# Kernel optimization log

Measured on AMD Instinct MI355X. Metric: run time of the kernel, lower is better.

The kernel has to match this reference:

```python
import jax, jax.numpy as jnp
import numpy as np

NUM_EXPERTS = 8
TOP_K = 2


def setup_inputs() -> dict:
    key = jax.random.key(0)
    ks = jax.random.split(key, 5)
    B, T, D, H, E = 8, 4096, 512, 1536, NUM_EXPERTS
    scale = 0.02
    x = jax.random.normal(ks[0], (B, T, D), dtype=jnp.float32)
    gate_w = jax.random.normal(ks[1], (E, D), dtype=jnp.float32) * scale
    w1 = jax.random.normal(ks[2], (E, H, D), dtype=jnp.float32) * scale
    w3 = jax.random.normal(ks[3], (E, H, D), dtype=jnp.float32) * scale
    w2 = jax.random.normal(ks[4], (E, D, H), dtype=jnp.float32) * scale
    return {"x": x, "gate_w": gate_w, "w1": w1, "w3": w3, "w2": w2}


def reference(x, gate_w, w1, w3, w2):
    B, T, D = x.shape
    E = gate_w.shape[0]
    xf = x.reshape(-1, D)                      # [N, D], N = B*T
    N = xf.shape[0]
    gate_logits = xf @ gate_w.T                # [N, E]
    weights, indices = jax.lax.top_k(gate_logits, TOP_K)   # [N, K]
    weights = jax.nn.softmax(weights, axis=-1)
    # combine[n, e] = sum_k weights[n, k] * (indices[n, k] == e)
    combine = jnp.zeros((N, E), dtype=xf.dtype).at[
        jnp.arange(N)[:, None], indices].add(weights)       # [N, E]
    out = jnp.zeros_like(xf)
    for e in range(E):  # small fixed expert count
        h = jax.nn.silu(xf @ w1[e].T) * (xf @ w3[e].T)      # [N, H]
        y = h @ w2[e].T                                     # [N, D]
        out = out + combine[:, e:e + 1] * y
    return out.reshape(B, T, D)
```

## Files before the change

### kernel.cpp

```cpp
#include <hip/hip_runtime.h>


#define N_TOK 32768
#define DIM   512
#define HID   1536
#define NE    8
#define MTS   256

typedef __attribute__((ext_vector_type(8))) short  short8;
typedef __attribute__((ext_vector_type(4))) float  floatx4;

#define MFMA(a,b,c) __builtin_amdgcn_mfma_f32_16x16x32_bf16(a,b,c,0,0,0)

__device__ __forceinline__ unsigned short f2bf(float f) {
  unsigned int u = __float_as_uint(f);
  u += 0x7fffu + ((u >> 16) & 1u);
  return (unsigned short)(u >> 16);
}
__device__ __forceinline__ unsigned pk2(float a, float b) {
  return (unsigned)f2bf(a) | ((unsigned)f2bf(b) << 16);
}
__device__ __forceinline__ void gl_lds16(const unsigned short* g, unsigned short* l) {
  __builtin_amdgcn_global_load_lds(
      (const __attribute__((address_space(1))) unsigned int*)g,
      (__attribute__((address_space(3))) unsigned int*)l, 16, 0, 0);
}

__global__ void __launch_bounds__(256) cvt_kernel(const float* __restrict__ src,
                                                  unsigned short* __restrict__ dst,
                                                  int n4) {
  int i = blockIdx.x * 256 + threadIdx.x;
  if (i >= n4) return;
  float4 v = ((const float4*)src)[i];
  uint2 o; o.x = pk2(v.x, v.y); o.y = pk2(v.z, v.w);
  ((uint2*)dst)[i] = o;
}

__global__ void __launch_bounds__(256) gate1_kernel(const float* __restrict__ x,
                                                    const float* __restrict__ gw,
                                                    unsigned short* __restrict__ xb,
                                                    unsigned* __restrict__ eidx,
                                                    float* __restrict__ wts) {
  int lane = threadIdx.x & 63;
  int wave = threadIdx.x >> 6;
  int t = blockIdx.x * 4 + wave;

  const float4* xp = (const float4*)(x + (size_t)t * DIM + lane * 8);
  float4 x0 = xp[0], x1 = xp[1];

  uint4 o; o.x = pk2(x0.x, x0.y); o.y = pk2(x0.z, x0.w);
  o.z = pk2(x1.x, x1.y); o.w = pk2(x1.z, x1.w);
  *(uint4*)(xb + (size_t)t * DIM + lane * 8) = o;

  double p[NE];
#pragma unroll
  for (int e = 0; e < NE; ++e) {
    const float4* gp = (const float4*)(gw + e * DIM + lane * 8);
    float4 g0 = gp[0], g1 = gp[1];
    p[e] = (double)x0.x * g0.x + (double)x0.y * g0.y + (double)x0.z * g0.z + (double)x0.w * g0.w
         + (double)x1.x * g1.x + (double)x1.y * g1.y + (double)x1.z * g1.z + (double)x1.w * g1.w;
  }
#pragma unroll
  for (int m = 1; m < 64; m <<= 1) {
#pragma unroll
    for (int e = 0; e < NE; ++e) p[e] += __shfl_xor(p[e], m);
  }
  if (lane == 0) {
    double m1 = -1e300, m2 = -1e300; int i1 = 0, i2 = 0;
#pragma unroll
    for (int e = 0; e < NE; ++e) {
      double v = p[e];
      if (v > m1) { m2 = m1; i2 = i1; m1 = v; i1 = e; }
      else if (v > m2) { m2 = v; i2 = e; }
    }
    float e2 = __expf((float)(m2 - m1));
    float wa = 1.f / (1.f + e2);
    eidx[t] = (unsigned)i1 | ((unsigned)i2 << 8);
    wts[t]  = wa;
  }
}

__global__ void __launch_bounds__(256) gate2_kernel(const unsigned* __restrict__ eidx,
                                                    const float* __restrict__ wts,
                                                    int* __restrict__ tokl,
                                                    float* __restrict__ wgtl,
                                                    int* __restrict__ cnt) {
  __shared__ unsigned hist[NE];
  __shared__ unsigned basep[NE];
  int tid = threadIdx.x;
  if (tid < NE) hist[tid] = 0;
  __syncthreads();
  int t0 = blockIdx.x * 1024;
  unsigned pk[4]; float wv[4];
#pragma unroll
  for (int i = 0; i < 4; ++i) {
    int t = t0 + tid + i * 256;
    pk[i] = eidx[t]; wv[i] = wts[t];
    atomicAdd(&hist[pk[i] & 0xff], 1u);
    atomicAdd(&hist[(pk[i] >> 8) & 0xff], 1u);
  }
  __syncthreads();
  if (tid < NE) {
    basep[tid] = (unsigned)atomicAdd(&cnt[tid], (int)hist[tid]);
    hist[tid] = 0;
  }
  __syncthreads();
#pragma unroll
  for (int i = 0; i < 4; ++i) {
    int t = t0 + tid + i * 256;
    int e1 = pk[i] & 0xff, e2 = (pk[i] >> 8) & 0xff;
    unsigned p1 = basep[e1] + atomicAdd(&hist[e1], 1u);
    tokl[e1 * N_TOK + p1] = t; wgtl[e1 * N_TOK + p1] = wv[i];
    unsigned p2 = basep[e2] + atomicAdd(&hist[e2], 1u);
    tokl[e2 * N_TOK + p2] = t | (int)0x80000000; wgtl[e2 * N_TOK + p2] = 1.f - wv[i];
  }
}

__global__ void __launch_bounds__(256, 4) ffn1_kernel(
    const unsigned short* __restrict__ xb,
    const unsigned short* __restrict__ w1b,
    const unsigned short* __restrict__ w3b,
    const int* __restrict__ tokl, const float* __restrict__ wgtl,
    const int* __restrict__ cnt,
    unsigned short* __restrict__ Hs,
    int h0base, int P, int NT) {
  int e  = blockIdx.x & 7;
  int t  = blockIdx.x >> 3;
  int nt = t % NT, mt = t / NT;
  int ne = cnt[e];
  int m0 = mt * 128;
  if (m0 >= ne) return;
  int offs = 0;
#pragma unroll
  for (int i = 0; i < NE; ++i) offs += (i < e) ? cnt[i] : 0;

  __shared__ __align__(16) unsigned short As[128 * 64];
  __shared__ __align__(16) unsigned short Bs[128 * 64];
  __shared__ float wgs[128];

  int tid = threadIdx.x, w = tid >> 6, lane = tid & 63;
  int quad = lane >> 4, l16 = lane & 15;
  int wm = w >> 1, wn = w & 1;

  if (tid < 128) {
    int r = m0 + tid;
    wgs[tid] = (r < ne) ? wgtl[e * N_TOK + r] : 0.f;
  }

  int rl = lane >> 3, cc = (lane & 7) ^ rl;
  const unsigned short* pa[4];
#pragma unroll
  for (int i = 0; i < 4; ++i) {
    int r = m0 + 32 * w + 8 * i + rl;
    int tok = tokl[e * N_TOK + (r < ne ? r : m0)] & 0x7fffffff;
    pa[i] = xb + (size_t)tok * DIM + cc * 8;
  }
  const unsigned short* wsrc = (w < 2) ? w1b : w3b;
  const unsigned short* pb0 =
      wsrc + ((size_t)e * HID + h0base + nt * 64 + ((32 * w) & 63) + rl) * DIM + cc * 8;

  floatx4 u[4][2], v[4][2];
#pragma unroll
  for (int i = 0; i < 4; ++i)
#pragma unroll
    for (int j = 0; j < 2; ++j) { u[i][j] = (floatx4){0,0,0,0}; v[i][j] = (floatx4){0,0,0,0}; }

  for (int k0 = 0; k0 < DIM; k0 += 64) {
#pragma unroll
    for (int i = 0; i < 4; ++i) {
      gl_lds16(pa[i], &As[(32 * w + 8 * i) * 64]);
      gl_lds16(pb0 + (size_t)i * 8 * DIM, &Bs[(32 * w + 8 * i) * 64]);
      pa[i] += 64;
    }
    pb0 += 64;
    __syncthreads();
#pragma unroll
    for (int kk = 0; kk < 2; ++kk) {
      int s = ((4 * kk + quad) ^ (l16 & 7)) * 8;
      short8 a[4], b1[2], b3[2];
#pragma unroll
      for (int i = 0; i < 4; ++i)
        a[i] = *(const short8*)&As[(wm * 64 + i * 16 + l16) * 64 + s];
#pragma unroll
      for (int j = 0; j < 2; ++j) {
        b1[j] = *(const short8*)&Bs[(wn * 32 + j * 16 + l16) * 64 + s];
        b3[j] = *(const short8*)&Bs[(64 + wn * 32 + j * 16 + l16) * 64 + s];
      }
#pragma unroll
      for (int i = 0; i < 4; ++i)
#pragma unroll
        for (int j = 0; j < 2; ++j) {
          u[i][j] = MFMA(a[i], b1[j], u[i][j]);
          v[i][j] = MFMA(a[i], b3[j], v[i][j]);
        }
    }
    __syncthreads();
  }

#pragma unroll
  for (int i = 0; i < 4; ++i)
#pragma unroll
    for (int j = 0; j < 2; ++j)
#pragma unroll
      for (int r = 0; r < 4; ++r) {
        int tr = wm * 64 + i * 16 + quad * 4 + r;
        int hc = wn * 32 + j * 16 + l16;
        float uu = u[i][j][r], vv = v[i][j][r];
        float h = (uu / (1.f + __expf(-uu))) * vv * wgs[tr];
        As[tr * 64 + hc] = f2bf(h);
      }
  __syncthreads();
  {
    int row = tid >> 1, half = tid & 1;
    if (m0 + row < ne) {
      const unsigned short* s = &As[row * 64 + half * 32];
      unsigned short* d = Hs + (size_t)(offs + m0 + row) * P + nt * 64 + half * 32;
#pragma unroll
      for (int j = 0; j < 4; ++j) *(uint4*)(d + j * 8) = *(const uint4*)(s + j * 8);
    }
  }
}

__global__ void __launch_bounds__(256, 4) ffn2_kernel(
    const unsigned short* __restrict__ Hs,
    const unsigned short* __restrict__ w2b,
    const int* __restrict__ tokl, const int* __restrict__ cnt,
    float* __restrict__ out, float* __restrict__ prt,
    int h0base, int P, int first) {
  int e  = blockIdx.x & 7;
  int t  = blockIdx.x >> 3;
  int nt = t & 3, mt = t >> 2;
  int ne = cnt[e];
  int m0 = mt * 128;
  if (m0 >= ne) return;
  int offs = 0;
#pragma unroll
  for (int i = 0; i < NE; ++i) offs += (i < e) ? cnt[i] : 0;

  __shared__ __align__(16) unsigned short As[128 * 64];
  __shared__ __align__(16) unsigned short Bs[128 * 64];
  __shared__ int toks[128];

  int tid = threadIdx.x, w = tid >> 6, lane = tid & 63;
  int quad = lane >> 4, l16 = lane & 15;
  int wm = w >> 1, wn = w & 1;
  if (tid < 128) { int r = m0 + tid; toks[tid] = tokl[e * N_TOK + (r < ne ? r : m0)]; }

  int rl = lane >> 3, cc = (lane & 7) ^ rl;
  int dbase = nt * 128;
  const unsigned short* pa0 = Hs + (size_t)(offs + m0 + 32 * w + rl) * P + cc * 8;
  const unsigned short* pb0 =
      w2b + ((size_t)e * DIM + dbase + 32 * w + rl) * HID + h0base + cc * 8;

  floatx4 acc[4][4];
#pragma unroll
  for (int i = 0; i < 4; ++i)
#pragma unroll
    for (int j = 0; j < 4; ++j) acc[i][j] = (floatx4){0,0,0,0};

  for (int k0 = 0; k0 < P; k0 += 64) {
#pragma unroll
    for (int i = 0; i < 4; ++i) {
      gl_lds16(pa0 + (size_t)i * 8 * P,   &As[(32 * w + 8 * i) * 64]);
      gl_lds16(pb0 + (size_t)i * 8 * HID, &Bs[(32 * w + 8 * i) * 64]);
    }
    pa0 += 64; pb0 += 64;
    __syncthreads();
#pragma unroll
    for (int kk = 0; kk < 2; ++kk) {
      int s = ((4 * kk + quad) ^ (l16 & 7)) * 8;
      short8 a[4], b[4];
#pragma unroll
      for (int i = 0; i < 4; ++i) {
        a[i] = *(const short8*)&As[(wm * 64 + i * 16 + l16) * 64 + s];
        b[i] = *(const short8*)&Bs[(wn * 64 + i * 16 + l16) * 64 + s];
      }
#pragma unroll
      for (int i = 0; i < 4; ++i)
#pragma unroll
        for (int j = 0; j < 4; ++j)
          acc[i][j] = MFMA(a[i], b[j], acc[i][j]);
    }
    __syncthreads();
  }

#pragma unroll
  for (int i = 0; i < 4; ++i)
#pragma unroll
    for (int r = 0; r < 4; ++r) {
      int row = wm * 64 + i * 16 + quad * 4 + r;
      if (m0 + row >= ne) continue;
      int tk = toks[row];
      float* dst = ((tk < 0) ? prt : out)
                   + (size_t)(tk & 0x7fffffff) * DIM + dbase + wn * 64 + l16;
      if (first) {
#pragma unroll
        for (int j = 0; j < 4; ++j) dst[j * 16] = acc[i][j][r];
      } else {
#pragma unroll
        for (int j = 0; j < 4; ++j) dst[j * 16] += acc[i][j][r];
      }
    }
}

__global__ void __launch_bounds__(256) combine_kernel(float* __restrict__ out,
                                                      const float* __restrict__ prt,
                                                      int n4) {
  for (int i = blockIdx.x * 256 + threadIdx.x; i < n4; i += gridDim.x * 256) {
    float4 a = ((const float4*)out)[i];
    float4 b = ((const float4*)prt)[i];
    a.x += b.x; a.y += b.y; a.z += b.z; a.w += b.w;
    ((float4*)out)[i] = a;
  }
}

extern "C" void kernel_launch(void* const* d_in, const int* in_sizes, int n_in,
                              void* d_out, int out_size, void* d_ws, size_t ws_size,
                              hipStream_t stream) {
  const float* x  = (const float*)d_in[0];
  const float* gw = (const float*)d_in[1];
  const float* w1 = (const float*)d_in[2];
  const float* w3 = (const float*)d_in[3];
  const float* w2 = (const float*)d_in[4];
  float* out = (float*)d_out;

  const size_t NW = (size_t)NE * HID * DIM;
  char* p = (char*)d_ws;
  unsigned short* w1b = (unsigned short*)p;  p += NW * 2;
  unsigned short* w3b = (unsigned short*)p;  p += NW * 2;
  unsigned short* w2b = (unsigned short*)p;  p += NW * 2;
  unsigned short* xb  = (unsigned short*)p;  p += (size_t)N_TOK * DIM * 2;
  int*      tokl = (int*)p;       p += (size_t)NE * N_TOK * 4;
  float*    wgtl = (float*)p;     p += (size_t)NE * N_TOK * 4;
  unsigned* eidx = (unsigned*)p;  p += (size_t)N_TOK * 4;
  float*    wts  = (float*)p;     p += (size_t)N_TOK * 4;
  int*      cnt  = (int*)p;       p += 256;
  float*    prt  = (float*)p;     p += (size_t)N_TOK * DIM * 4;
  unsigned short* Hs = (unsigned short*)p;
  size_t fixed = (size_t)(p - (char*)d_ws);
  if (ws_size < fixed) return;
  size_t avail = ws_size - fixed;

  const int cands[5] = {1536, 768, 512, 384, 256};
  int P = 0;
  for (int i = 0; i < 5; ++i)
    if ((size_t)(2 * N_TOK + 128) * cands[i] * 2 <= avail) { P = cands[i]; break; }
  if (!P) return;

  hipMemsetAsync(cnt, 0, NE * sizeof(int), stream);

  int n4 = (int)(NW / 4);
  cvt_kernel<<<n4 / 256, 256, 0, stream>>>(w1, w1b, n4);
  cvt_kernel<<<n4 / 256, 256, 0, stream>>>(w3, w3b, n4);
  cvt_kernel<<<n4 / 256, 256, 0, stream>>>(w2, w2b, n4);

  gate1_kernel<<<N_TOK / 4, 256, 0, stream>>>(x, gw, xb, eidx, wts);
  gate2_kernel<<<N_TOK / 1024, 256, 0, stream>>>(eidx, wts, tokl, wgtl, cnt);

  int pass = 0;
  for (int h0 = 0; h0 < HID; h0 += P) {
    int NT = P / 64;
    ffn1_kernel<<<8 * MTS * NT, 256, 0, stream>>>(xb, w1b, w3b, tokl, wgtl, cnt, Hs, h0, P, NT);
    ffn2_kernel<<<8 * MTS * 4, 256, 0, stream>>>(Hs, w2b, tokl, cnt, out, prt, h0, P, pass == 0);
    ++pass;
  }
  combine_kernel<<<2048, 256, 0, stream>>>(out, prt, N_TOK * DIM / 4);
}
```

Measured before the change: 686.6 us.

## Double-buffer LDS tiles in FFN kernels to overlap global loads with MFMA

```diff
diff --git a/kernel.cpp b/kernel.cpp
--- a/kernel.cpp
+++ b/kernel.cpp
@@ -116,7 +116,7 @@
   }
 }
 
-__global__ void __launch_bounds__(256, 4) ffn1_kernel(
+__global__ void __launch_bounds__(256, 2) ffn1_kernel(
     const unsigned short* __restrict__ xb,
     const unsigned short* __restrict__ w1b,
     const unsigned short* __restrict__ w3b,
@@ -134,8 +134,8 @@
 #pragma unroll
   for (int i = 0; i < NE; ++i) offs += (i < e) ? cnt[i] : 0;
 
-  __shared__ __align__(16) unsigned short As[128 * 64];
-  __shared__ __align__(16) unsigned short Bs[128 * 64];
+  __shared__ __align__(16) unsigned short As[2][128 * 64];
+  __shared__ __align__(16) unsigned short Bs[2][128 * 64];
   __shared__ float wgs[128];
 
   int tid = threadIdx.x, w = tid >> 6, lane = tid & 63;
@@ -159,32 +159,44 @@
   const unsigned short* pb0 =
       wsrc + ((size_t)e * HID + h0base + nt * 64 + ((32 * w) & 63) + rl) * DIM + cc * 8;
 
+  auto stage = [&](int b) {
+#pragma unroll
+    for (int i = 0; i < 4; ++i) {
+      gl_lds16(pa[i], &As[b][(32 * w + 8 * i) * 64]);
+      gl_lds16(pb0 + (size_t)i * 8 * DIM, &Bs[b][(32 * w + 8 * i) * 64]);
+      pa[i] += 64;
+    }
+    pb0 += 64;
+  };
+
   floatx4 u[4][2], v[4][2];
 #pragma unroll
   for (int i = 0; i < 4; ++i)
 #pragma unroll
     for (int j = 0; j < 2; ++j) { u[i][j] = (floatx4){0,0,0,0}; v[i][j] = (floatx4){0,0,0,0}; }
 
+  stage(0);
+  int cur = 0;
+#pragma unroll
   for (int k0 = 0; k0 < DIM; k0 += 64) {
-#pragma unroll
-    for (int i = 0; i < 4; ++i) {
-      gl_lds16(pa[i], &As[(32 * w + 8 * i) * 64]);
-      gl_lds16(pb0 + (size_t)i * 8 * DIM, &Bs[(32 * w + 8 * i) * 64]);
-      pa[i] += 64;
-    }
-    pb0 += 64;
-    __syncthreads();
+    if (k0 + 64 < DIM) {
+      stage(cur ^ 1);
+      asm volatile("s_waitcnt vmcnt(8)" ::: "memory");
+    } else {
+      asm volatile("s_waitcnt vmcnt(0)" ::: "memory");
+    }
+    __builtin_amdgcn_s_barrier();
 #pragma unroll
     for (int kk = 0; kk < 2; ++kk) {
       int s = ((4 * kk + quad) ^ (l16 & 7)) * 8;
       short8 a[4], b1[2], b3[2];
 #pragma unroll
       for (int i = 0; i < 4; ++i)
-        a[i] = *(const short8*)&As[(wm * 64 + i * 16 + l16) * 64 + s];
+        a[i] = *(const short8*)&As[cur][(wm * 64 + i * 16 + l16) * 64 + s];
 #pragma unroll
       for (int j = 0; j < 2; ++j) {
-        b1[j] = *(const short8*)&Bs[(wn * 32 + j * 16 + l16) * 64 + s];
-        b3[j] = *(const short8*)&Bs[(64 + wn * 32 + j * 16 + l16) * 64 + s];
+        b1[j] = *(const short8*)&Bs[cur][(wn * 32 + j * 16 + l16) * 64 + s];
+        b3[j] = *(const short8*)&Bs[cur][(64 + wn * 32 + j * 16 + l16) * 64 + s];
       }
 #pragma unroll
       for (int i = 0; i < 4; ++i)
@@ -194,7 +206,9 @@
           v[i][j] = MFMA(a[i], b3[j], v[i][j]);
         }
     }
-    __syncthreads();
+    asm volatile("" ::: "memory");
+    __builtin_amdgcn_s_barrier();
+    cur ^= 1;
   }
 
 #pragma unroll
@@ -207,13 +221,13 @@
         int hc = wn * 32 + j * 16 + l16;
         float uu = u[i][j][r], vv = v[i][j][r];
         float h = (uu / (1.f + __expf(-uu))) * vv * wgs[tr];
-        As[tr * 64 + hc] = f2bf(h);
+        As[0][tr * 64 + hc] = f2bf(h);
       }
   __syncthreads();
   {
     int row = tid >> 1, half = tid & 1;
     if (m0 + row < ne) {
-      const unsigned short* s = &As[row * 64 + half * 32];
+      const unsigned short* s = &As[0][row * 64 + half * 32];
       unsigned short* d = Hs + (size_t)(offs + m0 + row) * P + nt * 64 + half * 32;
 #pragma unroll
       for (int j = 0; j < 4; ++j) *(uint4*)(d + j * 8) = *(const uint4*)(s + j * 8);
@@ -221,7 +235,7 @@
   }
 }
 
-__global__ void __launch_bounds__(256, 4) ffn2_kernel(
+__global__ void __launch_bounds__(256, 2) ffn2_kernel(
     const unsigned short* __restrict__ Hs,
     const unsigned short* __restrict__ w2b,
     const int* __restrict__ tokl, const int* __restrict__ cnt,
@@ -237,8 +251,8 @@
 #pragma unroll
   for (int i = 0; i < NE; ++i) offs += (i < e) ? cnt[i] : 0;
 
-  __shared__ __align__(16) unsigned short As[128 * 64];
-  __shared__ __align__(16) unsigned short Bs[128 * 64];
+  __shared__ __align__(16) unsigned short As[2][128 * 64];
+  __shared__ __align__(16) unsigned short Bs[2][128 * 64];
   __shared__ int toks[128];
 
   int tid = threadIdx.x, w = tid >> 6, lane = tid & 63;
@@ -252,28 +266,39 @@
   const unsigned short* pb0 =
       w2b + ((size_t)e * DIM + dbase + 32 * w + rl) * HID + h0base + cc * 8;
 
+  auto stage = [&](int b) {
+#pragma unroll
+    for (int i = 0; i < 4; ++i) {
+      gl_lds16(pa0 + (size_t)i * 8 * P,   &As[b][(32 * w + 8 * i) * 64]);
+      gl_lds16(pb0 + (size_t)i * 8 * HID, &Bs[b][(32 * w + 8 * i) * 64]);
+    }
+    pa0 += 64; pb0 += 64;
+  };
+
   floatx4 acc[4][4];
 #pragma unroll
   for (int i = 0; i < 4; ++i)
 #pragma unroll
     for (int j = 0; j < 4; ++j) acc[i][j] = (floatx4){0,0,0,0};
 
+  stage(0);
+  int cur = 0;
   for (int k0 = 0; k0 < P; k0 += 64) {
-#pragma unroll
-    for (int i = 0; i < 4; ++i) {
-      gl_lds16(pa0 + (size_t)i * 8 * P,   &As[(32 * w + 8 * i) * 64]);
-      gl_lds16(pb0 + (size_t)i * 8 * HID, &Bs[(32 * w + 8 * i) * 64]);
-    }
-    pa0 += 64; pb0 += 64;
-    __syncthreads();
+    if (k0 + 64 < P) {
+      stage(cur ^ 1);
+      asm volatile("s_waitcnt vmcnt(8)" ::: "memory");
+    } else {
+      asm volatile("s_waitcnt vmcnt(0)" ::: "memory");
+    }
+    __builtin_amdgcn_s_barrier();
 #pragma unroll
     for (int kk = 0; kk < 2; ++kk) {
       int s = ((4 * kk + quad) ^ (l16 & 7)) * 8;
       short8 a[4], b[4];
 #pragma unroll
       for (int i = 0; i < 4; ++i) {
-        a[i] = *(const short8*)&As[(wm * 64 + i * 16 + l16) * 64 + s];
-        b[i] = *(const short8*)&Bs[(wn * 64 + i * 16 + l16) * 64 + s];
+        a[i] = *(const short8*)&As[cur][(wm * 64 + i * 16 + l16) * 64 + s];
+        b[i] = *(const short8*)&Bs[cur][(wn * 64 + i * 16 + l16) * 64 + s];
       }
 #pragma unroll
       for (int i = 0; i < 4; ++i)
@@ -281,7 +306,9 @@
         for (int j = 0; j < 4; ++j)
           acc[i][j] = MFMA(a[i], b[j], acc[i][j]);
     }
-    __syncthreads();
+    asm volatile("" ::: "memory");
+    __builtin_amdgcn_s_barrier();
+    cur ^= 1;
   }
 
 #pragma unroll
```

After: 753.9 us. 9.8% more time.

## Enlarge ffn1 tile to 256x128 with double-buffered LDS and staged prefetch

Applied to the files above, without the earlier changes.

```diff
diff --git a/kernel.cpp b/kernel.cpp
--- a/kernel.cpp
+++ b/kernel.cpp
@@ -6,11 +6,19 @@
 #define HID   1536
 #define NE    8
 #define MTS   256
+#define MT1   128
 
 typedef __attribute__((ext_vector_type(8))) short  short8;
 typedef __attribute__((ext_vector_type(4))) float  floatx4;
 
 #define MFMA(a,b,c) __builtin_amdgcn_mfma_f32_16x16x32_bf16(a,b,c,0,0,0)
+
+#define VMW4 asm volatile("s_waitcnt vmcnt(4)" ::: "memory")
+#define VMW2 asm volatile("s_waitcnt vmcnt(2)" ::: "memory")
+#define VMW0 asm volatile("s_waitcnt vmcnt(0)" ::: "memory")
+#define LG0  do { asm volatile("s_waitcnt lgkmcnt(0)" ::: "memory"); \
+                  __builtin_amdgcn_sched_barrier(0); } while (0)
+#define BARR __builtin_amdgcn_s_barrier()
 
 __device__ __forceinline__ unsigned short f2bf(float f) {
   unsigned int u = __float_as_uint(f);
@@ -116,7 +124,7 @@
   }
 }
 
-__global__ void __launch_bounds__(256, 4) ffn1_kernel(
+__global__ void __launch_bounds__(512, 2) ffn1_kernel(
     const unsigned short* __restrict__ xb,
     const unsigned short* __restrict__ w1b,
     const unsigned short* __restrict__ w3b,
@@ -128,95 +136,158 @@
   int t  = blockIdx.x >> 3;
   int nt = t % NT, mt = t / NT;
   int ne = cnt[e];
-  int m0 = mt * 128;
+  int m0 = mt * 256;
   if (m0 >= ne) return;
   int offs = 0;
 #pragma unroll
   for (int i = 0; i < NE; ++i) offs += (i < e) ? cnt[i] : 0;
 
-  __shared__ __align__(16) unsigned short As[128 * 64];
-  __shared__ __align__(16) unsigned short Bs[128 * 64];
-  __shared__ float wgs[128];
+  __shared__ __align__(16) unsigned short sA[2][256 * 64];
+  __shared__ __align__(16) unsigned short sB[2][256 * 64];
+  __shared__ float wgs[256];
 
   int tid = threadIdx.x, w = tid >> 6, lane = tid & 63;
   int quad = lane >> 4, l16 = lane & 15;
-  int wm = w >> 1, wn = w & 1;
-
-  if (tid < 128) {
+  int wm = w >> 2, wn = w & 3;
+  int rl = lane >> 3, c8 = lane & 7;
+  int sw = (c8 ^ rl) * 8;
+
+  if (tid < 256) {
     int r = m0 + tid;
     wgs[tid] = (r < ne) ? wgtl[e * N_TOK + r] : 0.f;
   }
 
-  int rl = lane >> 3, cc = (lane & 7) ^ rl;
-  const unsigned short* pa[4];
-#pragma unroll
-  for (int i = 0; i < 4; ++i) {
-    int r = m0 + 32 * w + 8 * i + rl;
-    int tok = tokl[e * N_TOK + (r < ne ? r : m0)] & 0x7fffffff;
-    pa[i] = xb + (size_t)tok * DIM + cc * 8;
-  }
-  const unsigned short* wsrc = (w < 2) ? w1b : w3b;
-  const unsigned short* pb0 =
-      wsrc + ((size_t)e * HID + h0base + nt * 64 + ((32 * w) & 63) + rl) * DIM + cc * 8;
-
-  floatx4 u[4][2], v[4][2];
-#pragma unroll
-  for (int i = 0; i < 4; ++i)
-#pragma unroll
-    for (int j = 0; j < 2; ++j) { u[i][j] = (floatx4){0,0,0,0}; v[i][j] = (floatx4){0,0,0,0}; }
-
-  for (int k0 = 0; k0 < DIM; k0 += 64) {
-#pragma unroll
-    for (int i = 0; i < 4; ++i) {
-      gl_lds16(pa[i], &As[(32 * w + 8 * i) * 64]);
-      gl_lds16(pb0 + (size_t)i * 8 * DIM, &Bs[(32 * w + 8 * i) * 64]);
-      pa[i] += 64;
-    }
-    pb0 += 64;
-    __syncthreads();
-#pragma unroll
-    for (int kk = 0; kk < 2; ++kk) {
-      int s = ((4 * kk + quad) ^ (l16 & 7)) * 8;
-      short8 a[4], b1[2], b3[2];
-#pragma unroll
-      for (int i = 0; i < 4; ++i)
-        a[i] = *(const short8*)&As[(wm * 64 + i * 16 + l16) * 64 + s];
+  const unsigned short* pa[2][2];
+#pragma unroll
+  for (int h = 0; h < 2; ++h)
+#pragma unroll
+    for (int ld = 0; ld < 2; ++ld) {
+      int row = h * 128 + ld * 64 + w * 8 + rl;
+      int rr = m0 + row;
+      int tok = tokl[e * N_TOK + (rr < ne ? rr : m0)] & 0x7fffffff;
+      pa[h][ld] = xb + (size_t)tok * DIM + sw;
+    }
+  const unsigned short* pb[2][2];
+#pragma unroll
+  for (int h = 0; h < 2; ++h)
+#pragma unroll
+    for (int ld = 0; ld < 2; ++ld) {
+      const unsigned short* ws = h ? w3b : w1b;
+      int hr = h0base + nt * 128 + ld * 64 + w * 8 + rl;
+      pb[h][ld] = ws + ((size_t)e * HID + hr) * DIM + sw;
+    }
+
+  auto stA = [&](int buf, int h, int kadd) {
+    unsigned short* d = &sA[buf][(h * 128 + w * 8) * 64];
+    gl_lds16(pa[h][0] + kadd, d);
+    gl_lds16(pa[h][1] + kadd, d + 64 * 64);
+  };
+  auto stB = [&](int buf, int h, int kadd) {
+    unsigned short* d = &sB[buf][(h * 128 + w * 8) * 64];
+    gl_lds16(pb[h][0] + kadd, d);
+    gl_lds16(pb[h][1] + kadd, d + 64 * 64);
+  };
+
+  short8 a[4][2], bu[2][2], bv[2][2];
+  floatx4 au[2][4][2], av[2][4][2];
+#pragma unroll
+  for (int mi = 0; mi < 2; ++mi)
+#pragma unroll
+    for (int i = 0; i < 4; ++i)
 #pragma unroll
       for (int j = 0; j < 2; ++j) {
-        b1[j] = *(const short8*)&Bs[(wn * 32 + j * 16 + l16) * 64 + s];
-        b3[j] = *(const short8*)&Bs[(64 + wn * 32 + j * 16 + l16) * 64 + s];
+        au[mi][i][j] = (floatx4){0, 0, 0, 0};
+        av[mi][i][j] = (floatx4){0, 0, 0, 0};
       }
-#pragma unroll
-      for (int i = 0; i < 4; ++i)
-#pragma unroll
-        for (int j = 0; j < 2; ++j) {
-          u[i][j] = MFMA(a[i], b1[j], u[i][j]);
-          v[i][j] = MFMA(a[i], b3[j], v[i][j]);
+
+  auto ldA = [&](int buf, int mi) {
+#pragma unroll
+    for (int i = 0; i < 4; ++i)
+#pragma unroll
+      for (int kk = 0; kk < 2; ++kk)
+        a[i][kk] = *(const short8*)&sA[buf][(wm * 128 + mi * 64 + i * 16 + l16) * 64 +
+                                           (((4 * kk + quad) ^ (l16 & 7)) * 8)];
+  };
+  auto ldB = [&](int buf, int h, short8 (&b)[2][2]) {
+#pragma unroll
+    for (int j = 0; j < 2; ++j)
+#pragma unroll
+      for (int kk = 0; kk < 2; ++kk)
+        b[j][kk] = *(const short8*)&sB[buf][(h * 128 + wn * 32 + j * 16 + l16) * 64 +
+                                           (((4 * kk + quad) ^ (l16 & 7)) * 8)];
+  };
+  auto mm = [&](short8 (&b)[2][2], floatx4 (&ac)[4][2]) {
+    __builtin_amdgcn_s_setprio(1);
+#pragma unroll
+    for (int i = 0; i < 4; ++i)
+#pragma unroll
+      for (int j = 0; j < 2; ++j)
+#pragma unroll
+        for (int kk = 0; kk < 2; ++kk)
+          ac[i][j] = MFMA(a[i][kk], b[j][kk], ac[i][j]);
+    __builtin_amdgcn_s_setprio(0);
+  };
+
+  stA(0, 0, 0); stA(0, 1, 0); stB(0, 0, 0); stB(0, 1, 0);
+
+  int cur = 0;
+  for (int tt = 0; tt < (DIM / 64) - 1; ++tt) {
+    int kadd = (tt + 1) * 64;
+    int nx = cur ^ 1;
+    stA(nx, 0, kadd);
+    VMW4; BARR;
+    ldA(cur, 0); ldB(cur, 0, bu);
+    LG0; mm(bu, au[0]); BARR;
+    stA(nx, 1, kadd);
+    VMW4; BARR;
+    ldB(cur, 1, bv);
+    LG0; mm(bv, av[0]); BARR;
+    stB(nx, 0, kadd);
+    BARR;
+    ldA(cur, 1);
+    LG0; mm(bu, au[1]); BARR;
+    stB(nx, 1, kadd);
+    BARR;
+    mm(bv, av[1]); BARR;
+    cur = nx;
+  }
+  VMW2; BARR;
+  ldA(cur, 0); ldB(cur, 0, bu);
+  LG0; mm(bu, au[0]); BARR;
+  VMW0; BARR;
+  ldB(cur, 1, bv);
+  LG0; mm(bv, av[0]); BARR;
+  BARR;
+  ldA(cur, 1);
+  LG0; mm(bu, au[1]); BARR;
+  mm(bv, av[1]);
+  __syncthreads();
+
+  unsigned short* AsF = &sA[0][0];
+#pragma unroll
+  for (int mi = 0; mi < 2; ++mi)
+#pragma unroll
+    for (int i = 0; i < 4; ++i)
+#pragma unroll
+      for (int j = 0; j < 2; ++j)
+#pragma unroll
+        for (int r = 0; r < 4; ++r) {
+          int tr = wm * 128 + mi * 64 + i * 16 + quad * 4 + r;
+          int hc = wn * 32 + j * 16 + l16;
+          float uu = au[mi][i][j][r], vv = av[mi][i][j][r];
+          float h = (uu / (1.f + __expf(-uu))) * vv * wgs[tr];
+          AsF[tr * 128 + hc] = f2bf(h);
         }
-    }
-    __syncthreads();
-  }
-
-#pragma unroll
-  for (int i = 0; i < 4; ++i)
-#pragma unroll
-    for (int j = 0; j < 2; ++j)
-#pragma unroll
-      for (int r = 0; r < 4; ++r) {
-        int tr = wm * 64 + i * 16 + quad * 4 + r;
-        int hc = wn * 32 + j * 16 + l16;
-        float uu = u[i][j][r], vv = v[i][j][r];
-        float h = (uu / (1.f + __expf(-uu))) * vv * wgs[tr];
-        As[tr * 64 + hc] = f2bf(h);
-      }
   __syncthreads();
   {
-    int row = tid >> 1, half = tid & 1;
-    if (m0 + row < ne) {
-      const unsigned short* s = &As[row * 64 + half * 32];
-      unsigned short* d = Hs + (size_t)(offs + m0 + row) * P + nt * 64 + half * 32;
-#pragma unroll
-      for (int j = 0; j < 4; ++j) *(uint4*)(d + j * 8) = *(const uint4*)(s + j * 8);
+#pragma unroll
+    for (int ro = 0; ro < 8; ++ro) {
+      int row = ro * 32 + (tid >> 4);
+      int ch = (tid & 15) * 8;
+      if (m0 + row < ne) {
+        *(uint4*)(Hs + (size_t)(offs + m0 + row) * P + nt * 128 + ch) =
+            *(const uint4*)(AsF + row * 128 + ch);
+      }
     }
   }
 }
@@ -256,7 +327,7 @@
 #pragma unroll
   for (int i = 0; i < 4; ++i)
 #pragma unroll
-    for (int j = 0; j < 4; ++j) acc[i][j] = (floatx4){0,0,0,0};
+    for (int j = 0; j < 4; ++j) acc[i][j] = (floatx4){0, 0, 0, 0};
 
   for (int k0 = 0; k0 < P; k0 += 64) {
 #pragma unroll
@@ -359,8 +430,8 @@
 
   int pass = 0;
   for (int h0 = 0; h0 < HID; h0 += P) {
-    int NT = P / 64;
-    ffn1_kernel<<<8 * MTS * NT, 256, 0, stream>>>(xb, w1b, w3b, tokl, wgtl, cnt, Hs, h0, P, NT);
+    int NT1 = P / 128;
+    ffn1_kernel<<<8 * MT1 * NT1, 512, 0, stream>>>(xb, w1b, w3b, tokl, wgtl, cnt, Hs, h0, P, NT1);
     ffn2_kernel<<<8 * MTS * 4, 256, 0, stream>>>(Hs, w2b, tokl, cnt, out, prt, h0, P, pass == 0);
     ++pass;
   }
```

Result: no change. 686.5 us (-0.0%).

## Drop partial-output buffer by sorting primary/secondary rows and splitting ffn2 passes

Applied to the files above, without the earlier changes.

```diff
diff --git a/kernel.cpp b/kernel.cpp
--- a/kernel.cpp
+++ b/kernel.cpp
@@ -26,14 +26,21 @@
       (__attribute__((address_space(3))) unsigned int*)l, 16, 0, 0);
 }
 
-__global__ void __launch_bounds__(256) cvt_kernel(const float* __restrict__ src,
-                                                  unsigned short* __restrict__ dst,
-                                                  int n4) {
+__global__ void __launch_bounds__(256) cvt3_kernel(const float* __restrict__ w1,
+                                                   const float* __restrict__ w3,
+                                                   const float* __restrict__ w2,
+                                                   unsigned short* __restrict__ w1b,
+                                                   unsigned short* __restrict__ w3b,
+                                                   unsigned short* __restrict__ w2b,
+                                                   int n4) {
   int i = blockIdx.x * 256 + threadIdx.x;
-  if (i >= n4) return;
-  float4 v = ((const float4*)src)[i];
+  const float* s; unsigned short* d; int j = i;
+  if (j < n4)          { s = w1; d = w1b; }
+  else if (j < 2 * n4) { s = w3; d = w3b; j -= n4; }
+  else                 { s = w2; d = w2b; j -= 2 * n4; }
+  float4 v = ((const float4*)s)[j];
   uint2 o; o.x = pk2(v.x, v.y); o.y = pk2(v.z, v.w);
-  ((uint2*)dst)[i] = o;
+  ((uint2*)d)[j] = o;
 }
 
 __global__ void __launch_bounds__(256) gate1_kernel(const float* __restrict__ x,
@@ -80,15 +87,35 @@
   }
 }
 
-__global__ void __launch_bounds__(256) gate2_kernel(const unsigned* __restrict__ eidx,
-                                                    const float* __restrict__ wts,
-                                                    int* __restrict__ tokl,
-                                                    float* __restrict__ wgtl,
-                                                    int* __restrict__ cnt) {
-  __shared__ unsigned hist[NE];
-  __shared__ unsigned basep[NE];
+__global__ void __launch_bounds__(256) gate2a_kernel(const unsigned* __restrict__ eidx,
+                                                     int* __restrict__ cnt) {
+  __shared__ unsigned histP[NE], histS[NE];
   int tid = threadIdx.x;
-  if (tid < NE) hist[tid] = 0;
+  if (tid < NE) { histP[tid] = 0; histS[tid] = 0; }
+  __syncthreads();
+  int t0 = blockIdx.x * 1024;
+#pragma unroll
+  for (int i = 0; i < 4; ++i) {
+    unsigned pk = eidx[t0 + tid + i * 256];
+    atomicAdd(&histP[pk & 0xff], 1u);
+    atomicAdd(&histS[(pk >> 8) & 0xff], 1u);
+  }
+  __syncthreads();
+  if (tid < NE) {
+    atomicAdd(&cnt[tid], (int)histP[tid]);
+    atomicAdd(&cnt[NE + tid], (int)histS[tid]);
+  }
+}
+
+__global__ void __launch_bounds__(256) gate2b_kernel(const unsigned* __restrict__ eidx,
+                                                     const float* __restrict__ wts,
+                                                     int* __restrict__ tokl,
+                                                     float* __restrict__ wgtl,
+                                                     int* __restrict__ cnt) {
+  __shared__ unsigned histP[NE], histS[NE];
+  __shared__ unsigned baseP[NE], baseS[NE];
+  int tid = threadIdx.x;
+  if (tid < NE) { histP[tid] = 0; histS[tid] = 0; }
   __syncthreads();
   int t0 = blockIdx.x * 1024;
   unsigned pk[4]; float wv[4];
@@ -96,27 +123,28 @@
   for (int i = 0; i < 4; ++i) {
     int t = t0 + tid + i * 256;
     pk[i] = eidx[t]; wv[i] = wts[t];
-    atomicAdd(&hist[pk[i] & 0xff], 1u);
-    atomicAdd(&hist[(pk[i] >> 8) & 0xff], 1u);
+    atomicAdd(&histP[pk[i] & 0xff], 1u);
+    atomicAdd(&histS[(pk[i] >> 8) & 0xff], 1u);
   }
   __syncthreads();
   if (tid < NE) {
-    basep[tid] = (unsigned)atomicAdd(&cnt[tid], (int)hist[tid]);
-    hist[tid] = 0;
+    baseP[tid] = (unsigned)atomicAdd(&cnt[2 * NE + tid], (int)histP[tid]);
+    baseS[tid] = (unsigned)cnt[tid] + (unsigned)atomicAdd(&cnt[3 * NE + tid], (int)histS[tid]);
+    histP[tid] = 0; histS[tid] = 0;
   }
   __syncthreads();
 #pragma unroll
   for (int i = 0; i < 4; ++i) {
     int t = t0 + tid + i * 256;
     int e1 = pk[i] & 0xff, e2 = (pk[i] >> 8) & 0xff;
-    unsigned p1 = basep[e1] + atomicAdd(&hist[e1], 1u);
+    unsigned p1 = baseP[e1] + atomicAdd(&histP[e1], 1u);
     tokl[e1 * N_TOK + p1] = t; wgtl[e1 * N_TOK + p1] = wv[i];
-    unsigned p2 = basep[e2] + atomicAdd(&hist[e2], 1u);
+    unsigned p2 = baseS[e2] + atomicAdd(&histS[e2], 1u);
     tokl[e2 * N_TOK + p2] = t | (int)0x80000000; wgtl[e2 * N_TOK + p2] = 1.f - wv[i];
   }
 }
 
-__global__ void __launch_bounds__(256, 4) ffn1_kernel(
+__global__ void __launch_bounds__(256, 5) ffn1_kernel(
     const unsigned short* __restrict__ xb,
     const unsigned short* __restrict__ w1b,
     const unsigned short* __restrict__ w3b,
@@ -127,25 +155,19 @@
   int e  = blockIdx.x & 7;
   int t  = blockIdx.x >> 3;
   int nt = t % NT, mt = t / NT;
-  int ne = cnt[e];
+  int ne = cnt[e] + cnt[NE + e];
   int m0 = mt * 128;
   if (m0 >= ne) return;
   int offs = 0;
 #pragma unroll
-  for (int i = 0; i < NE; ++i) offs += (i < e) ? cnt[i] : 0;
+  for (int i = 0; i < NE; ++i) offs += (i < e) ? (cnt[i] + cnt[NE + i]) : 0;
 
   __shared__ __align__(16) unsigned short As[128 * 64];
   __shared__ __align__(16) unsigned short Bs[128 * 64];
-  __shared__ float wgs[128];
 
   int tid = threadIdx.x, w = tid >> 6, lane = tid & 63;
   int quad = lane >> 4, l16 = lane & 15;
   int wm = w >> 1, wn = w & 1;
-
-  if (tid < 128) {
-    int r = m0 + tid;
-    wgs[tid] = (r < ne) ? wgtl[e * N_TOK + r] : 0.f;
-  }
 
   int rl = lane >> 3, cc = (lane & 7) ^ rl;
   const unsigned short* pa[4];
@@ -200,15 +222,17 @@
 #pragma unroll
   for (int i = 0; i < 4; ++i)
 #pragma unroll
-    for (int j = 0; j < 2; ++j)
-#pragma unroll
-      for (int r = 0; r < 4; ++r) {
-        int tr = wm * 64 + i * 16 + quad * 4 + r;
+    for (int r = 0; r < 4; ++r) {
+      int tr = wm * 64 + i * 16 + quad * 4 + r;
+      float wg = wgtl[e * N_TOK + m0 + tr];
+#pragma unroll
+      for (int j = 0; j < 2; ++j) {
         int hc = wn * 32 + j * 16 + l16;
         float uu = u[i][j][r], vv = v[i][j][r];
-        float h = (uu / (1.f + __expf(-uu))) * vv * wgs[tr];
+        float h = (uu / (1.f + __expf(-uu))) * vv * wg;
         As[tr * 64 + hc] = f2bf(h);
       }
+    }
   __syncthreads();
   {
     int row = tid >> 1, half = tid & 1;
@@ -221,30 +245,30 @@
   }
 }
 
-__global__ void __launch_bounds__(256, 4) ffn2_kernel(
+__global__ void __launch_bounds__(256, 5) ffn2_kernel(
     const unsigned short* __restrict__ Hs,
     const unsigned short* __restrict__ w2b,
     const int* __restrict__ tokl, const int* __restrict__ cnt,
-    float* __restrict__ out, float* __restrict__ prt,
-    int h0base, int P, int first) {
+    float* __restrict__ out,
+    int h0base, int P, int first, int cls) {
   int e  = blockIdx.x & 7;
   int t  = blockIdx.x >> 3;
   int nt = t & 3, mt = t >> 2;
-  int ne = cnt[e];
+  int neP = cnt[e];
+  int neAll = neP + cnt[NE + e];
   int m0 = mt * 128;
-  if (m0 >= ne) return;
+  if (cls == 0) { if (m0 >= neP) return; }
+  else          { if (m0 >= neAll || m0 + 128 <= neP) return; }
   int offs = 0;
 #pragma unroll
-  for (int i = 0; i < NE; ++i) offs += (i < e) ? cnt[i] : 0;
+  for (int i = 0; i < NE; ++i) offs += (i < e) ? (cnt[i] + cnt[NE + i]) : 0;
 
   __shared__ __align__(16) unsigned short As[128 * 64];
   __shared__ __align__(16) unsigned short Bs[128 * 64];
-  __shared__ int toks[128];
 
   int tid = threadIdx.x, w = tid >> 6, lane = tid & 63;
   int quad = lane >> 4, l16 = lane & 15;
   int wm = w >> 1, wn = w & 1;
-  if (tid < 128) { int r = m0 + tid; toks[tid] = tokl[e * N_TOK + (r < ne ? r : m0)]; }
 
   int rl = lane >> 3, cc = (lane & 7) ^ rl;
   int dbase = nt * 128;
@@ -256,7 +280,7 @@
 #pragma unroll
   for (int i = 0; i < 4; ++i)
 #pragma unroll
-    for (int j = 0; j < 4; ++j) acc[i][j] = (floatx4){0,0,0,0};
+    for (int j = 0; j < 4; ++j) acc[i][j] = (floatx4){0, 0, 0, 0};
 
   for (int k0 = 0; k0 < P; k0 += 64) {
 #pragma unroll
@@ -289,11 +313,12 @@
 #pragma unroll
     for (int r = 0; r < 4; ++r) {
       int row = wm * 64 + i * 16 + quad * 4 + r;
-      if (m0 + row >= ne) continue;
-      int tk = toks[row];
-      float* dst = ((tk < 0) ? prt : out)
-                   + (size_t)(tk & 0x7fffffff) * DIM + dbase + wn * 64 + l16;
-      if (first) {
+      int gr = m0 + row;
+      int tk = tokl[e * N_TOK + gr];
+      bool doit = cls ? (gr < neAll && tk < 0) : (gr < neP);
+      if (!doit) continue;
+      float* dst = out + (size_t)(tk & 0x7fffffff) * DIM + dbase + wn * 64 + l16;
+      if (first && cls == 0) {
 #pragma unroll
         for (int j = 0; j < 4; ++j) dst[j * 16] = acc[i][j][r];
       } else {
@@ -301,17 +326,6 @@
         for (int j = 0; j < 4; ++j) dst[j * 16] += acc[i][j][r];
       }
     }
-}
-
-__global__ void __launch_bounds__(256) combine_kernel(float* __restrict__ out,
-                                                      const float* __restrict__ prt,
-                                                      int n4) {
-  for (int i = blockIdx.x * 256 + threadIdx.x; i < n4; i += gridDim.x * 256) {
-    float4 a = ((const float4*)out)[i];
-    float4 b = ((const float4*)prt)[i];
-    a.x += b.x; a.y += b.y; a.z += b.z; a.w += b.w;
-    ((float4*)out)[i] = a;
-  }
 }
 
 extern "C" void kernel_launch(void* const* d_in, const int* in_sizes, int n_in,
@@ -335,7 +349,6 @@
   unsigned* eidx = (unsigned*)p;  p += (size_t)N_TOK * 4;
   float*    wts  = (float*)p;     p += (size_t)N_TOK * 4;
   int*      cnt  = (int*)p;       p += 256;
-  float*    prt  = (float*)p;     p += (size_t)N_TOK * DIM * 4;
   unsigned short* Hs = (unsigned short*)p;
   size_t fixed = (size_t)(p - (char*)d_ws);
   if (ws_size < fixed) return;
@@ -347,22 +360,21 @@
     if ((size_t)(2 * N_TOK + 128) * cands[i] * 2 <= avail) { P = cands[i]; break; }
   if (!P) return;
 
-  hipMemsetAsync(cnt, 0, NE * sizeof(int), stream);
+  hipMemsetAsync(cnt, 0, 256, stream);
 
   int n4 = (int)(NW / 4);
-  cvt_kernel<<<n4 / 256, 256, 0, stream>>>(w1, w1b, n4);
-  cvt_kernel<<<n4 / 256, 256, 0, stream>>>(w3, w3b, n4);
-  cvt_kernel<<<n4 / 256, 256, 0, stream>>>(w2, w2b, n4);
+  cvt3_kernel<<<3 * n4 / 256, 256, 0, stream>>>(w1, w3, w2, w1b, w3b, w2b, n4);
 
   gate1_kernel<<<N_TOK / 4, 256, 0, stream>>>(x, gw, xb, eidx, wts);
-  gate2_kernel<<<N_TOK / 1024, 256, 0, stream>>>(eidx, wts, tokl, wgtl, cnt);
+  gate2a_kernel<<<N_TOK / 1024, 256, 0, stream>>>(eidx, cnt);
+  gate2b_kernel<<<N_TOK / 1024, 256, 0, stream>>>(eidx, wts, tokl, wgtl, cnt);
 
   int pass = 0;
   for (int h0 = 0; h0 < HID; h0 += P) {
     int NT = P / 64;
     ffn1_kernel<<<8 * MTS * NT, 256, 0, stream>>>(xb, w1b, w3b, tokl, wgtl, cnt, Hs, h0, P, NT);
-    ffn2_kernel<<<8 * MTS * 4, 256, 0, stream>>>(Hs, w2b, tokl, cnt, out, prt, h0, P, pass == 0);
+    ffn2_kernel<<<8 * MTS * 4, 256, 0, stream>>>(Hs, w2b, tokl, cnt, out, h0, P, pass == 0, 0);
+    ffn2_kernel<<<8 * MTS * 4, 256, 0, stream>>>(Hs, w2b, tokl, cnt, out, h0, P, 0, 1);
     ++pass;
   }
-  combine_kernel<<<2048, 256, 0, stream>>>(out, prt, N_TOK * DIM / 4);
-}
+}
```

After: 1.369 ms. +99.4%, slower.
